# Kernel tuning notes

Hardware: AMD Instinct MI355X
Metric: run time of the kernel (lower is better)

## Reference

```python
import jax, jax.numpy as jnp
import numpy as np

N, E = 50000, 800000          # nodes, edges
CUR, HID, OUT = 128, 128, 128  # cur_dim, hidden_dim, output_dim
NEG_SLOPE = 0.01               # F.leaky_relu default


def setup_inputs() -> dict:
    key = jax.random.key(0)
    ks = jax.random.split(key, 12)
    rn = lambda k, shp, s: jax.random.normal(k, shp, dtype=jnp.float32) * s
    s_c, s_h, s_o = 1.0 / np.sqrt(CUR), 1.0 / np.sqrt(HID), 1.0 / np.sqrt(OUT)
    return {
        "h": rn(ks[0], (N, CUR), 1.0),
        "x": rn(ks[1], (N, CUR), 1.0),
        "edge_index": jax.random.randint(ks[2], (2, E), 0, N, dtype=jnp.int32),
        "edge_weight": jax.random.uniform(ks[3], (E,), dtype=jnp.float32),
        # preprocessor_x: Linear(CUR, HID)
        "Wp": rn(ks[4], (HID, CUR), s_c), "bp": jnp.zeros((HID,), jnp.float32),
        # ChebConv(HID, OUT, K=2): two weight mats + bias
        "Wc0": rn(ks[5], (OUT, HID), s_h), "Wc1": rn(ks[6], (OUT, HID), s_h),
        "bc": jnp.zeros((OUT,), jnp.float32),
        # SAGEConv(HID, OUT): lin_rel (neighbors, with bias) + lin_root (self)
        "Wrel": rn(ks[7], (OUT, HID), s_h), "brel": jnp.zeros((OUT,), jnp.float32),
        "Wroot": rn(ks[8], (OUT, HID), s_h),
        # final Linear(OUT, OUT)
        "Wl": rn(ks[9], (OUT, OUT), s_o), "bl": jnp.zeros((OUT,), jnp.float32),
    }


def reference(h, x, edge_index, edge_weight, Wp, bp, Wc0, Wc1, bc,
              Wrel, brel, Wroot, Wl, bl):
    n = x.shape[0]
    src, dst = edge_index[0], edge_index[1]
    seg = lambda d, i: jax.ops.segment_sum(d, i, num_segments=n)

    his = x
    xh = x @ Wp.T + bp                               # [N, HID]

    # --- ChebConv, K=2, sym norm, lambda_max=2 => Lhat = -D^{-1/2} A D^{-1/2}
    deg = seg(edge_weight, src)                       # weighted degree
    dis = jnp.where(deg > 0, jax.lax.rsqrt(jnp.where(deg > 0, deg, 1.0)), 0.0)
    norm = -dis[src] * edge_weight * dis[dst]         # [E]
    Tx1 = seg(norm[:, None] * xh[src], dst)           # [N, HID]
    o1 = jax.nn.leaky_relu(xh @ Wc0.T + Tx1 @ Wc1.T + bc, NEG_SLOPE)

    # --- SAGEConv: mean of edge_weight-scaled neighbor feats + root transform
    msum = seg(edge_weight[:, None] * xh[src], dst)   # [N, HID]
    cnt = seg(jnp.ones_like(edge_weight), dst)        # in-degree
    mean = msum / jnp.maximum(cnt, 1.0)[:, None]
    o2 = jax.nn.leaky_relu(mean @ Wrel.T + brel + xh @ Wroot.T, NEG_SLOPE)

    o3 = (o1 + o2) @ Wl.T + bl
    return (his, o3)
```

## Files before the change

kernel.cpp:

```cpp
#include <hip/hip_runtime.h>

#define NN 50000
#define EE 800000
#define D  128
#define NCH 64
#define CH  12500
#define NR  8
#define RS  6250
#define KCB 512
#define XHB 782
#define CSB 196
#define PKB 384
#define FB  391

typedef short short8 __attribute__((ext_vector_type(8)));
typedef float floatx4 __attribute__((ext_vector_type(4)));
typedef float floatx16 __attribute__((ext_vector_type(16)));

__device__ __forceinline__ float leaky(float v) { return v > 0.f ? v : 0.01f * v; }

__device__ __forceinline__ unsigned short f2bf(float f) {
    unsigned int u = __float_as_uint(f);
    u = (u + 0x7fff + ((u >> 16) & 1)) >> 16;
    return (unsigned short)u;
}
__device__ __forceinline__ float bf2f(unsigned int h) {
    return __uint_as_float(h << 16);
}

__global__ __launch_bounds__(256) void k_pre(
    const float* __restrict__ Wp,  const float* __restrict__ Wc0,
    const float* __restrict__ Wc1, const float* __restrict__ Wrel,
    const float* __restrict__ Wroot, const float* __restrict__ Wl,
    unsigned short* __restrict__ Pall) {
    int gid = blockIdx.x * 256 + threadIdx.x;
    int mm = gid >> 14;
    int r = gid & 16383;
    int j  = r & 7;
    int l  = (r >> 3) & 63;
    int n, k;
    if (mm == 0) {
        int ct = (r >> 9) & 7;
        int kc = r >> 12;
        n = ct * 16 + (l & 15);
        k = kc * 32 + (l >> 4) * 8 + j;
    } else {
        int ct = (r >> 9) & 3;
        int kc = (r >> 11) & 7;
        n = ct * 32 + (l & 31);
        k = kc * 16 + (l >> 5) * 8 + j;
    }
    const float* W = mm == 0 ? Wp : mm == 1 ? Wc0 : mm == 2 ? Wc1
                   : mm == 3 ? Wrel : mm == 4 ? Wroot : Wl;
    Pall[gid] = f2bf(W[n * 128 + k]);
}

__global__ __launch_bounds__(256) void k_main(
    const int* __restrict__ src, const int* __restrict__ dst,
    const float* __restrict__ ew,
    int* __restrict__ counts,
    float* __restrict__ degp,
    unsigned short* __restrict__ rank,
    const float* __restrict__ x, const float* __restrict__ bp,
    unsigned short* __restrict__ xh16, float* __restrict__ his,
    const unsigned short* __restrict__ Pall) {
    __shared__ int   scnt[RS];
    __shared__ float sdeg[RS];
    int b = blockIdx.x;
    if (b < KCB) {
        int c = b & 63;
        int rge = b >> 6;
        int rlo = rge * RS;
        for (int i = threadIdx.x; i < RS; i += 256) { scnt[i] = 0; sdeg[i] = 0.f; }
        __syncthreads();
        int base = c * CH;
        for (int i0 = threadIdx.x * 4; i0 < CH; i0 += 1024) {
            int e = base + i0;
            int4   s4 = *(const int4*)(src + e);
            int4   d4 = *(const int4*)(dst + e);
            float4 w4 = *(const float4*)(ew + e);
            unsigned dr, sr;
            dr = (unsigned)(d4.x - rlo);
            if (dr < RS) rank[e]     = (unsigned short)atomicAdd(&scnt[dr], 1);
            sr = (unsigned)(s4.x - rlo);
            if (sr < RS) atomicAdd(&sdeg[sr], w4.x);
            dr = (unsigned)(d4.y - rlo);
            if (dr < RS) rank[e + 1] = (unsigned short)atomicAdd(&scnt[dr], 1);
            sr = (unsigned)(s4.y - rlo);
            if (sr < RS) atomicAdd(&sdeg[sr], w4.y);
            dr = (unsigned)(d4.z - rlo);
            if (dr < RS) rank[e + 2] = (unsigned short)atomicAdd(&scnt[dr], 1);
            sr = (unsigned)(s4.z - rlo);
            if (sr < RS) atomicAdd(&sdeg[sr], w4.z);
            dr = (unsigned)(d4.w - rlo);
            if (dr < RS) rank[e + 3] = (unsigned short)atomicAdd(&scnt[dr], 1);
            sr = (unsigned)(s4.w - rlo);
            if (sr < RS) atomicAdd(&sdeg[sr], w4.w);
        }
        __syncthreads();
        size_t ob = (size_t)c * NN + rlo;
        for (int i = threadIdx.x; i < RS; i += 256) {
            counts[ob + i] = scnt[i];
            degp[ob + i]   = sdeg[i];
        }
    } else {
        int bb = b - KCB;
        const unsigned short* Pp = Pall;
        int wave = threadIdx.x >> 6, l = threadIdx.x & 63;
        int n0 = bb * 64 + wave * 16;
        int m = l & 15, q = l >> 4;
        int nodeA = n0 + m;
        bool av = nodeA < NN;
        int na = av ? nodeA : 0;
        floatx4 acc[8];
#pragma unroll
        for (int ct = 0; ct < 8; ++ct) acc[ct] = (floatx4)(0.f);
#pragma unroll
        for (int kc = 0; kc < 4; ++kc) {
            const float* ap = x + (size_t)na * 128 + kc * 32 + q * 8;
            float4 f0 = av ? *(const float4*)ap       : make_float4(0, 0, 0, 0);
            float4 f1 = av ? *(const float4*)(ap + 4) : make_float4(0, 0, 0, 0);
            if (av) {
                float* hp = his + (size_t)nodeA * 128 + kc * 32 + q * 8;
                *(float4*)hp       = f0;
                *(float4*)(hp + 4) = f1;
            }
            short8 a;
            a[0] = f2bf(f0.x); a[1] = f2bf(f0.y); a[2] = f2bf(f0.z); a[3] = f2bf(f0.w);
            a[4] = f2bf(f1.x); a[5] = f2bf(f1.y); a[6] = f2bf(f1.z); a[7] = f2bf(f1.w);
#pragma unroll
            for (int ct = 0; ct < 8; ++ct) {
                short8 bfr = *(const short8*)(Pp + ((kc * 8 + ct) << 9) + l * 8);
                acc[ct] = __builtin_amdgcn_mfma_f32_16x16x32_bf16(a, bfr, acc[ct], 0, 0, 0);
            }
        }
#pragma unroll
        for (int ct = 0; ct < 8; ++ct) {
            int col = ct * 16 + m;
            float bias = bp[col];
#pragma unroll
            for (int r = 0; r < 4; ++r) {
                int node = n0 + q * 4 + r;
                if (node < NN) xh16[(size_t)node * 128 + col] = f2bf(acc[ct][r] + bias);
            }
        }
    }
}

__global__ __launch_bounds__(256) void k_colscan(int* __restrict__ counts,
                                                 const float* __restrict__ degp,
                                                 int* __restrict__ cntI,
                                                 float* __restrict__ deg,
                                                 int* __restrict__ blocksum) {
    __shared__ int ws4[4];
    int t = threadIdx.x;
    int n = blockIdx.x * 256 + t;
    int acc = 0; float dacc = 0.f;
    if (n < NN) {
#pragma unroll 8
        for (int c = 0; c < NCH; ++c) {
            size_t idx = (size_t)c * NN + n;
            int v = counts[idx];
            counts[idx] = acc;
            acc += v;
            dacc += degp[idx];
        }
        cntI[n] = acc;
        deg[n] = dacc;
    }
    int s = (n < NN) ? acc : 0;
#pragma unroll
    for (int off = 32; off > 0; off >>= 1) s += __shfl_down(s, off, 64);
    if ((t & 63) == 0) ws4[t >> 6] = s;
    __syncthreads();
    if (t == 0) blocksum[blockIdx.x] = ws4[0] + ws4[1] + ws4[2] + ws4[3];
}

__global__ __launch_bounds__(256) void k_scan_mid(const int* __restrict__ blocksum,
                                                  int* __restrict__ blockoff,
                                                  int* __restrict__ rowstart) {
    __shared__ int wtot[4];
    int t = threadIdx.x, lane = t & 63, wave = t >> 6;
    int v = (t < CSB) ? blocksum[t] : 0;
    int incl = v;
#pragma unroll
    for (int off = 1; off < 64; off <<= 1) {
        int u = __shfl_up(incl, off, 64);
        if (lane >= off) incl += u;
    }
    if (lane == 63) wtot[wave] = incl;
    __syncthreads();
    int wpre = 0;
    for (int w = 0; w < wave; ++w) wpre += wtot[w];
    incl += wpre;
    if (t < CSB) blockoff[t] = incl - v;
    if (t == 255) rowstart[NN] = incl;
}

__global__ __launch_bounds__(256) void k_scan_final(const int* __restrict__ cntI,
                                                    const int* __restrict__ blockoff,
                                                    int* __restrict__ rowstart) {
    __shared__ int wtot[4];
    int t = threadIdx.x, lane = t & 63, wave = t >> 6;
    int n = blockIdx.x * 256 + t;
    int v = (n < NN) ? cntI[n] : 0;
    int incl = v;
#pragma unroll
    for (int off = 1; off < 64; off <<= 1) {
        int u = __shfl_up(incl, off, 64);
        if (lane >= off) incl += u;
    }
    if (lane == 63) wtot[wave] = incl;
    __syncthreads();
    int wpre = 0;
    for (int w = 0; w < wave; ++w) wpre += wtot[w];
    incl += wpre;
    if (n < NN) rowstart[n] = blockoff[blockIdx.x] + incl - v;
}

__global__ __launch_bounds__(256) void k_bucket(const int* __restrict__ src,
                                                const int* __restrict__ dst,
                                                const float* __restrict__ ew,
                                                const float* __restrict__ deg,
                                                const int* __restrict__ rowstart,
                                                const int* __restrict__ chunkoff,
                                                const unsigned short* __restrict__ rank,
                                                int4* __restrict__ rec) {
    int e = blockIdx.x * blockDim.x + threadIdx.x;
    if (e >= EE) return;
    int s = src[e], d = dst[e];
    float w = ew[e];
    float degs = deg[s];
    float dis_s = degs > 0.f ? rsqrtf(degs) : 0.f;
    int c = e / CH;
    int pos = rowstart[d] + chunkoff[(size_t)c * NN + d] + (int)rank[e];
    int4 r;
    r.x = s;
    r.y = __float_as_int(w);
    r.z = __float_as_int(dis_s * w);
    r.w = 0;
    rec[pos] = r;
}

__global__ __launch_bounds__(256) void k_gather(const int* __restrict__ rowstart,
                                                const int4* __restrict__ rec,
                                                const float* __restrict__ deg,
                                                const unsigned short* __restrict__ xh16,
                                                unsigned int* __restrict__ tx16,
                                                unsigned int* __restrict__ mn16) {
    int wave = threadIdx.x >> 6, l = threadIdx.x & 63;
    int n = blockIdx.x * 4 + wave;
    if (n >= NN) return;
    int lo = rowstart[n], hi = rowstart[n + 1];
    float at0 = 0.f, at1 = 0.f, am0 = 0.f, am1 = 0.f;
    int e = lo;
    for (; e + 3 < hi; e += 4) {
        int4 r0 = rec[e], r1 = rec[e + 1], r2 = rec[e + 2], r3 = rec[e + 3];
        unsigned int v0 = *(const unsigned int*)(xh16 + (size_t)r0.x * 128 + l * 2);
        unsigned int v1 = *(const unsigned int*)(xh16 + (size_t)r1.x * 128 + l * 2);
        unsigned int v2 = *(const unsigned int*)(xh16 + (size_t)r2.x * 128 + l * 2);
        unsigned int v3 = *(const unsigned int*)(xh16 + (size_t)r3.x * 128 + l * 2);
        float w0 = __int_as_float(r0.y), u0 = __int_as_float(r0.z);
        float w1 = __int_as_float(r1.y), u1 = __int_as_float(r1.z);
        float w2 = __int_as_float(r2.y), u2 = __int_as_float(r2.z);
        float w3 = __int_as_float(r3.y), u3 = __int_as_float(r3.z);
        float a0 = bf2f(v0 & 0xffff), a1 = bf2f(v0 >> 16);
        float b0 = bf2f(v1 & 0xffff), b1 = bf2f(v1 >> 16);
        float c0 = bf2f(v2 & 0xffff), c1 = bf2f(v2 >> 16);
        float d0 = bf2f(v3 & 0xffff), d1 = bf2f(v3 >> 16);
        am0 = fmaf(w0, a0, am0); am1 = fmaf(w0, a1, am1);
        at0 = fmaf(u0, a0, at0); at1 = fmaf(u0, a1, at1);
        am0 = fmaf(w1, b0, am0); am1 = fmaf(w1, b1, am1);
        at0 = fmaf(u1, b0, at0); at1 = fmaf(u1, b1, at1);
        am0 = fmaf(w2, c0, am0); am1 = fmaf(w2, c1, am1);
        at0 = fmaf(u2, c0, at0); at1 = fmaf(u2, c1, at1);
        am0 = fmaf(w3, d0, am0); am1 = fmaf(w3, d1, am1);
        at0 = fmaf(u3, d0, at0); at1 = fmaf(u3, d1, at1);
    }
    for (; e < hi; ++e) {
        int4 r0 = rec[e];
        unsigned int v0 = *(const unsigned int*)(xh16 + (size_t)r0.x * 128 + l * 2);
        float w0 = __int_as_float(r0.y), u0 = __int_as_float(r0.z);
        float a0 = bf2f(v0 & 0xffff), a1 = bf2f(v0 >> 16);
        am0 = fmaf(w0, a0, am0); am1 = fmaf(w0, a1, am1);
        at0 = fmaf(u0, a0, at0); at1 = fmaf(u0, a1, at1);
    }
    float dd = deg[n];
    float dis_d = dd > 0.f ? rsqrtf(dd) : 0.f;
    int c = hi - lo;
    float ic = 1.f / (float)(c > 0 ? c : 1);
    unsigned int tpack = (unsigned int)f2bf(-dis_d * at0) |
                         ((unsigned int)f2bf(-dis_d * at1) << 16);
    unsigned int mpack = (unsigned int)f2bf(am0 * ic) |
                         ((unsigned int)f2bf(am1 * ic) << 16);
    tx16[(size_t)n * 64 + l] = tpack;
    mn16[(size_t)n * 64 + l] = mpack;
}

__global__ __launch_bounds__(256, 2) void k_fused(const unsigned short* __restrict__ xh16,
                                               const unsigned short* __restrict__ tx16,
                                               const unsigned short* __restrict__ mn16,
                                               const unsigned short* __restrict__ Pall,
                                               const float* __restrict__ bc,
                                               const float* __restrict__ brel,
                                               const float* __restrict__ bl,
                                               float* __restrict__ out) {
    const unsigned short* Pc0  = Pall + 1 * 16384;
    const unsigned short* Pc1  = Pall + 2 * 16384;
    const unsigned short* Prel = Pall + 3 * 16384;
    const unsigned short* Proot= Pall + 4 * 16384;
    const unsigned short* Pl   = Pall + 5 * 16384;
    __shared__ __align__(16) unsigned short sS[4][32][128];
    int w = threadIdx.x >> 6, l = threadIdx.x & 63;
    int n0 = blockIdx.x * 128 + w * 32;
    int row = l & 31, half = l >> 5;
    int node = n0 + row;
    bool av = node < NN;
    size_t ra = (size_t)(av ? node : 0) * 128 + half * 8;
    short8 Axh[8], Atx[8], Amn[8];
#pragma unroll
    for (int kc = 0; kc < 8; ++kc) {
        Axh[kc] = *(const short8*)(xh16 + ra + kc * 16);
        Atx[kc] = *(const short8*)(tx16 + ra + kc * 16);
        Amn[kc] = *(const short8*)(mn16 + ra + kc * 16);
    }
#pragma unroll
    for (int ct = 0; ct < 4; ++ct) {
        floatx16 acc1 = (floatx16)(0.f), acc2 = (floatx16)(0.f);
#pragma unroll
        for (int kc = 0; kc < 8; ++kc) {
            int po = ((kc * 4 + ct) << 9) + l * 8;
            short8 b0 = *(const short8*)(Pc0 + po);
            short8 b1 = *(const short8*)(Pc1 + po);
            short8 b2 = *(const short8*)(Prel + po);
            short8 b3 = *(const short8*)(Proot + po);
            acc1 = __builtin_amdgcn_mfma_f32_32x32x16_bf16(Axh[kc], b0, acc1, 0, 0, 0);
            acc1 = __builtin_amdgcn_mfma_f32_32x32x16_bf16(Atx[kc], b1, acc1, 0, 0, 0);
            acc2 = __builtin_amdgcn_mfma_f32_32x32x16_bf16(Amn[kc], b2, acc2, 0, 0, 0);
            acc2 = __builtin_amdgcn_mfma_f32_32x32x16_bf16(Axh[kc], b3, acc2, 0, 0, 0);
        }
        int col = ct * 32 + row;
        float b1v = bc[col], b2v = brel[col];
#pragma unroll
        for (int r = 0; r < 16; ++r) {
            int rr = (r & 3) + 8 * (r >> 2) + 4 * half;
            float u = leaky(acc1[r] + b1v) + leaky(acc2[r] + b2v);
            int sw = ((((col >> 3) ^ rr) & 15) << 3) | (col & 7);
            sS[w][rr][sw] = f2bf(u);
        }
    }
    short8 As[8];
#pragma unroll
    for (int kc = 0; kc < 8; ++kc) {
        int g = (kc * 2 + half) ^ (row & 15);
        As[kc] = *(const short8*)&sS[w][row][g << 3];
    }
#pragma unroll
    for (int ct = 0; ct < 4; ++ct) {
        floatx16 acc3 = (floatx16)(0.f);
#pragma unroll
        for (int kc = 0; kc < 8; ++kc) {
            short8 b = *(const short8*)(Pl + ((kc * 4 + ct) << 9) + l * 8);
            acc3 = __builtin_amdgcn_mfma_f32_32x32x16_bf16(As[kc], b, acc3, 0, 0, 0);
        }
        int col = ct * 32 + row;
        float bv = bl[col];
#pragma unroll
        for (int r = 0; r < 16; ++r) {
            int rr = (r & 3) + 8 * (r >> 2) + 4 * half;
            int nd = n0 + rr;
            if (nd < NN) out[(size_t)nd * 128 + col] = acc3[r] + bv;
        }
    }
}

extern "C" void kernel_launch(void* const* d_in, const int* in_sizes, int n_in,
                              void* d_out, int out_size, void* d_ws, size_t ws_size,
                              hipStream_t stream) {
    const float* x    = (const float*)d_in[1];
    const int*   ei   = (const int*)d_in[2];
    const float* ew   = (const float*)d_in[3];
    const float* Wp   = (const float*)d_in[4];
    const float* bp   = (const float*)d_in[5];
    const float* Wc0  = (const float*)d_in[6];
    const float* Wc1  = (const float*)d_in[7];
    const float* bc   = (const float*)d_in[8];
    const float* Wrel = (const float*)d_in[9];
    const float* brel = (const float*)d_in[10];
    const float* Wroot= (const float*)d_in[11];
    const float* Wl   = (const float*)d_in[12];
    const float* bl   = (const float*)d_in[13];
    (void)in_sizes; (void)n_in; (void)out_size; (void)ws_size;
    float* out = (float*)d_out;

    unsigned short* xh16 = (unsigned short*)d_ws;
    unsigned short* tx16 = xh16 + (size_t)NN * 128;
    unsigned short* mn16 = tx16 + (size_t)NN * 128;
    unsigned short* Pall = mn16 + (size_t)NN * 128;
    int*   counts = (int*)(Pall + 6 * 16384);
    int4*  rec    = (int4*)(counts + (size_t)NCH * NN);
    float* degp   = (float*)rec;
    unsigned short* rank = (unsigned short*)(rec + EE);
    int*   rowstart = (int*)(rank + EE);
    int*   blocksum = rowstart + NN + 2;
    int*   blockoff = blocksum + CSB;
    int*   cntI   = blockoff + CSB;
    float* deg    = (float*)(cntI + NN);

    const int* srcI = ei;
    const int* dstI = ei + EE;

    k_pre<<<PKB, 256, 0, stream>>>(Wp, Wc0, Wc1, Wrel, Wroot, Wl, Pall);
    k_main<<<KCB + XHB, 256, 0, stream>>>(
        srcI, dstI, ew, counts, degp, rank, x, bp, xh16, out, Pall);
    k_colscan<<<CSB, 256, 0, stream>>>(counts, degp, cntI, deg, blocksum);
    k_scan_mid<<<1, 256, 0, stream>>>(blocksum, blockoff, rowstart);
    k_scan_final<<<CSB, 256, 0, stream>>>(cntI, blockoff, rowstart);
    k_bucket<<<(EE + 255) / 256, 256, 0, stream>>>(srcI, dstI, ew, deg, rowstart,
                                                   counts, rank, rec);
    k_gather<<<(NN + 3) / 4, 256, 0, stream>>>(rowstart, rec, deg, xh16,
                                               (unsigned int*)tx16, (unsigned int*)mn16);
    k_fused<<<FB, 256, 0, stream>>>(xh16, tx16, mn16, Pall,
                                    bc, brel, bl, out + (size_t)NN * 128);
}
```

Measured before the change: 266.0 us.

## Split gather edges across half-waves and distribute fused GEMM column tiles across waves

The gather kernel now has each half-wave take alternate edges and load 4 bf16 features per lane, then combines the halves with a cross-half shuffle. Each half then writes one of the two outputs. The fused MLP kernel gives each block 32 nodes and assigns one 32-column tile to each of its four waves, sharing the intermediate through LDS with a barrier. This raises the block count and occupancy (launch bounds 4) and lowers per-wave register pressure. The costs are that each wave now loads the activation rows redundantly and a __syncthreads is added.

```diff
diff --git a/kernel.cpp b/kernel.cpp
--- a/kernel.cpp
+++ b/kernel.cpp
@@ -11,7 +11,7 @@
 #define XHB 782
 #define CSB 196
 #define PKB 384
-#define FB  391
+#define FB  1563
 
 typedef short short8 __attribute__((ext_vector_type(8)));
 typedef float floatx4 __attribute__((ext_vector_type(4)));
@@ -252,52 +252,79 @@
     int n = blockIdx.x * 4 + wave;
     if (n >= NN) return;
     int lo = rowstart[n], hi = rowstart[n + 1];
-    float at0 = 0.f, at1 = 0.f, am0 = 0.f, am1 = 0.f;
-    int e = lo;
-    for (; e + 3 < hi; e += 4) {
-        int4 r0 = rec[e], r1 = rec[e + 1], r2 = rec[e + 2], r3 = rec[e + 3];
-        unsigned int v0 = *(const unsigned int*)(xh16 + (size_t)r0.x * 128 + l * 2);
-        unsigned int v1 = *(const unsigned int*)(xh16 + (size_t)r1.x * 128 + l * 2);
-        unsigned int v2 = *(const unsigned int*)(xh16 + (size_t)r2.x * 128 + l * 2);
-        unsigned int v3 = *(const unsigned int*)(xh16 + (size_t)r3.x * 128 + l * 2);
+    int half = l >> 5, c32 = l & 31;
+    float am0 = 0.f, am1 = 0.f, am2 = 0.f, am3 = 0.f;
+    float at0 = 0.f, at1 = 0.f, at2 = 0.f, at3 = 0.f;
+    int e = lo + half;
+    for (; e + 6 < hi; e += 8) {
+        int4 r0 = rec[e], r1 = rec[e + 2], r2 = rec[e + 4], r3 = rec[e + 6];
+        uint2 v0 = *(const uint2*)(xh16 + (size_t)r0.x * 128 + c32 * 4);
+        uint2 v1 = *(const uint2*)(xh16 + (size_t)r1.x * 128 + c32 * 4);
+        uint2 v2 = *(const uint2*)(xh16 + (size_t)r2.x * 128 + c32 * 4);
+        uint2 v3 = *(const uint2*)(xh16 + (size_t)r3.x * 128 + c32 * 4);
         float w0 = __int_as_float(r0.y), u0 = __int_as_float(r0.z);
         float w1 = __int_as_float(r1.y), u1 = __int_as_float(r1.z);
         float w2 = __int_as_float(r2.y), u2 = __int_as_float(r2.z);
         float w3 = __int_as_float(r3.y), u3 = __int_as_float(r3.z);
-        float a0 = bf2f(v0 & 0xffff), a1 = bf2f(v0 >> 16);
-        float b0 = bf2f(v1 & 0xffff), b1 = bf2f(v1 >> 16);
-        float c0 = bf2f(v2 & 0xffff), c1 = bf2f(v2 >> 16);
-        float d0 = bf2f(v3 & 0xffff), d1 = bf2f(v3 >> 16);
+        float a0, a1, a2, a3;
+        a0 = bf2f(v0.x & 0xffff); a1 = bf2f(v0.x >> 16);
+        a2 = bf2f(v0.y & 0xffff); a3 = bf2f(v0.y >> 16);
         am0 = fmaf(w0, a0, am0); am1 = fmaf(w0, a1, am1);
+        am2 = fmaf(w0, a2, am2); am3 = fmaf(w0, a3, am3);
         at0 = fmaf(u0, a0, at0); at1 = fmaf(u0, a1, at1);
-        am0 = fmaf(w1, b0, am0); am1 = fmaf(w1, b1, am1);
-        at0 = fmaf(u1, b0, at0); at1 = fmaf(u1, b1, at1);
-        am0 = fmaf(w2, c0, am0); am1 = fmaf(w2, c1, am1);
-        at0 = fmaf(u2, c0, at0); at1 = fmaf(u2, c1, at1);
-        am0 = fmaf(w3, d0, am0); am1 = fmaf(w3, d1, am1);
-        at0 = fmaf(u3, d0, at0); at1 = fmaf(u3, d1, at1);
-    }
-    for (; e < hi; ++e) {
+        at2 = fmaf(u0, a2, at2); at3 = fmaf(u0, a3, at3);
+        a0 = bf2f(v1.x & 0xffff); a1 = bf2f(v1.x >> 16);
+        a2 = bf2f(v1.y & 0xffff); a3 = bf2f(v1.y >> 16);
+        am0 = fmaf(w1, a0, am0); am1 = fmaf(w1, a1, am1);
+        am2 = fmaf(w1, a2, am2); am3 = fmaf(w1, a3, am3);
+        at0 = fmaf(u1, a0, at0); at1 = fmaf(u1, a1, at1);
+        at2 = fmaf(u1, a2, at2); at3 = fmaf(u1, a3, at3);
+        a0 = bf2f(v2.x & 0xffff); a1 = bf2f(v2.x >> 16);
+        a2 = bf2f(v2.y & 0xffff); a3 = bf2f(v2.y >> 16);
+        am0 = fmaf(w2, a0, am0); am1 = fmaf(w2, a1, am1);
+        am2 = fmaf(w2, a2, am2); am3 = fmaf(w2, a3, am3);
+        at0 = fmaf(u2, a0, at0); at1 = fmaf(u2, a1, at1);
+        at2 = fmaf(u2, a2, at2); at3 = fmaf(u2, a3, at3);
+        a0 = bf2f(v3.x & 0xffff); a1 = bf2f(v3.x >> 16);
+        a2 = bf2f(v3.y & 0xffff); a3 = bf2f(v3.y >> 16);
+        am0 = fmaf(w3, a0, am0); am1 = fmaf(w3, a1, am1);
+        am2 = fmaf(w3, a2, am2); am3 = fmaf(w3, a3, am3);
+        at0 = fmaf(u3, a0, at0); at1 = fmaf(u3, a1, at1);
+        at2 = fmaf(u3, a2, at2); at3 = fmaf(u3, a3, at3);
+    }
+    for (; e < hi; e += 2) {
         int4 r0 = rec[e];
-        unsigned int v0 = *(const unsigned int*)(xh16 + (size_t)r0.x * 128 + l * 2);
+        uint2 v0 = *(const uint2*)(xh16 + (size_t)r0.x * 128 + c32 * 4);
         float w0 = __int_as_float(r0.y), u0 = __int_as_float(r0.z);
-        float a0 = bf2f(v0 & 0xffff), a1 = bf2f(v0 >> 16);
+        float a0 = bf2f(v0.x & 0xffff), a1 = bf2f(v0.x >> 16);
+        float a2 = bf2f(v0.y & 0xffff), a3 = bf2f(v0.y >> 16);
         am0 = fmaf(w0, a0, am0); am1 = fmaf(w0, a1, am1);
+        am2 = fmaf(w0, a2, am2); am3 = fmaf(w0, a3, am3);
         at0 = fmaf(u0, a0, at0); at1 = fmaf(u0, a1, at1);
-    }
+        at2 = fmaf(u0, a2, at2); at3 = fmaf(u0, a3, at3);
+    }
+    am0 += __shfl_xor(am0, 32, 64); am1 += __shfl_xor(am1, 32, 64);
+    am2 += __shfl_xor(am2, 32, 64); am3 += __shfl_xor(am3, 32, 64);
+    at0 += __shfl_xor(at0, 32, 64); at1 += __shfl_xor(at1, 32, 64);
+    at2 += __shfl_xor(at2, 32, 64); at3 += __shfl_xor(at3, 32, 64);
     float dd = deg[n];
     float dis_d = dd > 0.f ? rsqrtf(dd) : 0.f;
     int c = hi - lo;
     float ic = 1.f / (float)(c > 0 ? c : 1);
-    unsigned int tpack = (unsigned int)f2bf(-dis_d * at0) |
-                         ((unsigned int)f2bf(-dis_d * at1) << 16);
-    unsigned int mpack = (unsigned int)f2bf(am0 * ic) |
-                         ((unsigned int)f2bf(am1 * ic) << 16);
-    tx16[(size_t)n * 64 + l] = tpack;
-    mn16[(size_t)n * 64 + l] = mpack;
-}
-
-__global__ __launch_bounds__(256, 2) void k_fused(const unsigned short* __restrict__ xh16,
+    if (half == 0) {
+        uint2 t;
+        t.x = (unsigned int)f2bf(-dis_d * at0) | ((unsigned int)f2bf(-dis_d * at1) << 16);
+        t.y = (unsigned int)f2bf(-dis_d * at2) | ((unsigned int)f2bf(-dis_d * at3) << 16);
+        *(uint2*)(tx16 + (size_t)n * 64 + c32 * 2) = t;
+    } else {
+        uint2 m;
+        m.x = (unsigned int)f2bf(am0 * ic) | ((unsigned int)f2bf(am1 * ic) << 16);
+        m.y = (unsigned int)f2bf(am2 * ic) | ((unsigned int)f2bf(am3 * ic) << 16);
+        *(uint2*)(mn16 + (size_t)n * 64 + c32 * 2) = m;
+    }
+}
+
+__global__ __launch_bounds__(256, 4) void k_fused(const unsigned short* __restrict__ xh16,
                                                const unsigned short* __restrict__ tx16,
                                                const unsigned short* __restrict__ mn16,
                                                const unsigned short* __restrict__ Pall,
@@ -310,67 +337,53 @@
     const unsigned short* Prel = Pall + 3 * 16384;
     const unsigned short* Proot= Pall + 4 * 16384;
     const unsigned short* Pl   = Pall + 5 * 16384;
-    __shared__ __align__(16) unsigned short sS[4][32][128];
-    int w = threadIdx.x >> 6, l = threadIdx.x & 63;
-    int n0 = blockIdx.x * 128 + w * 32;
+    __shared__ __align__(16) unsigned short sS[32][128];
+    int ct = threadIdx.x >> 6, l = threadIdx.x & 63;
+    int n0 = blockIdx.x * 32;
     int row = l & 31, half = l >> 5;
     int node = n0 + row;
     bool av = node < NN;
     size_t ra = (size_t)(av ? node : 0) * 128 + half * 8;
-    short8 Axh[8], Atx[8], Amn[8];
+    floatx16 acc1 = (floatx16)(0.f), acc2 = (floatx16)(0.f);
 #pragma unroll
     for (int kc = 0; kc < 8; ++kc) {
-        Axh[kc] = *(const short8*)(xh16 + ra + kc * 16);
-        Atx[kc] = *(const short8*)(tx16 + ra + kc * 16);
-        Amn[kc] = *(const short8*)(mn16 + ra + kc * 16);
-    }
-#pragma unroll
-    for (int ct = 0; ct < 4; ++ct) {
-        floatx16 acc1 = (floatx16)(0.f), acc2 = (floatx16)(0.f);
-#pragma unroll
-        for (int kc = 0; kc < 8; ++kc) {
-            int po = ((kc * 4 + ct) << 9) + l * 8;
-            short8 b0 = *(const short8*)(Pc0 + po);
-            short8 b1 = *(const short8*)(Pc1 + po);
-            short8 b2 = *(const short8*)(Prel + po);
-            short8 b3 = *(const short8*)(Proot + po);
-            acc1 = __builtin_amdgcn_mfma_f32_32x32x16_bf16(Axh[kc], b0, acc1, 0, 0, 0);
-            acc1 = __builtin_amdgcn_mfma_f32_32x32x16_bf16(Atx[kc], b1, acc1, 0, 0, 0);
-            acc2 = __builtin_amdgcn_mfma_f32_32x32x16_bf16(Amn[kc], b2, acc2, 0, 0, 0);
-            acc2 = __builtin_amdgcn_mfma_f32_32x32x16_bf16(Axh[kc], b3, acc2, 0, 0, 0);
-        }
-        int col = ct * 32 + row;
-        float b1v = bc[col], b2v = brel[col];
-#pragma unroll
-        for (int r = 0; r < 16; ++r) {
-            int rr = (r & 3) + 8 * (r >> 2) + 4 * half;
-            float u = leaky(acc1[r] + b1v) + leaky(acc2[r] + b2v);
-            int sw = ((((col >> 3) ^ rr) & 15) << 3) | (col & 7);
-            sS[w][rr][sw] = f2bf(u);
-        }
-    }
-    short8 As[8];
+        short8 Axh = *(const short8*)(xh16 + ra + kc * 16);
+        short8 Atx = *(const short8*)(tx16 + ra + kc * 16);
+        short8 Amn = *(const short8*)(mn16 + ra + kc * 16);
+        int po = ((kc * 4 + ct) << 9) + l * 8;
+        short8 b0 = *(const short8*)(Pc0 + po);
+        short8 b1 = *(const short8*)(Pc1 + po);
+        short8 b2 = *(const short8*)(Prel + po);
+        short8 b3 = *(const short8*)(Proot + po);
+        acc1 = __builtin_amdgcn_mfma_f32_32x32x16_bf16(Axh, b0, acc1, 0, 0, 0);
+        acc1 = __builtin_amdgcn_mfma_f32_32x32x16_bf16(Atx, b1, acc1, 0, 0, 0);
+        acc2 = __builtin_amdgcn_mfma_f32_32x32x16_bf16(Amn, b2, acc2, 0, 0, 0);
+        acc2 = __builtin_amdgcn_mfma_f32_32x32x16_bf16(Axh, b3, acc2, 0, 0, 0);
+    }
+    int col = ct * 32 + row;
+    float b1v = bc[col], b2v = brel[col];
+#pragma unroll
+    for (int r = 0; r < 16; ++r) {
+        int rr = (r & 3) + 8 * (r >> 2) + 4 * half;
+        float u = leaky(acc1[r] + b1v) + leaky(acc2[r] + b2v);
+        int sw = ((((col >> 3) ^ rr) & 15) << 3) | (col & 7);
+        sS[rr][sw] = f2bf(u);
+    }
+    __syncthreads();
+    floatx16 acc3 = (floatx16)(0.f);
 #pragma unroll
     for (int kc = 0; kc < 8; ++kc) {
         int g = (kc * 2 + half) ^ (row & 15);
-        As[kc] = *(const short8*)&sS[w][row][g << 3];
-    }
-#pragma unroll
-    for (int ct = 0; ct < 4; ++ct) {
-        floatx16 acc3 = (floatx16)(0.f);
-#pragma unroll
-        for (int kc = 0; kc < 8; ++kc) {
-            short8 b = *(const short8*)(Pl + ((kc * 4 + ct) << 9) + l * 8);
-            acc3 = __builtin_amdgcn_mfma_f32_32x32x16_bf16(As[kc], b, acc3, 0, 0, 0);
-        }
-        int col = ct * 32 + row;
-        float bv = bl[col];
-#pragma unroll
-        for (int r = 0; r < 16; ++r) {
-            int rr = (r & 3) + 8 * (r >> 2) + 4 * half;
-            int nd = n0 + rr;
-            if (nd < NN) out[(size_t)nd * 128 + col] = acc3[r] + bv;
-        }
+        short8 As = *(const short8*)&sS[row][g << 3];
+        short8 b = *(const short8*)(Pl + ((kc * 4 + ct) << 9) + l * 8);
+        acc3 = __builtin_amdgcn_mfma_f32_32x32x16_bf16(As, b, acc3, 0, 0, 0);
+    }
+    float bv = bl[col];
+#pragma unroll
+    for (int r = 0; r < 16; ++r) {
+        int rr = (r & 3) + 8 * (r >> 2) + 4 * half;
+        int nd = n0 + rr;
+        if (nd < NN) out[(size_t)nd * 128 + col] = acc3[r] + bv;
     }
 }
 
```

Measured after the change: 257.5 us. 3.2% less time.
